# Performance work log

Measured on AMD Instinct MI355X. Metric: run time of the kernel, lower is better.

The kernel has to match this reference:

```python
import jax, jax.numpy as jnp
import numpy as np
from jax import lax

# dims
B, CH, CC, DG, H, W = 2, 256, 256, 8, 64, 64
KK = 3  # dcn kernel size
K = KK * KK
GN_GROUPS = 32
EPS = 1e-6


def conv2d(x, w, b, pad=0, groups=1):
    out = lax.conv_general_dilated(x, w, (1, 1), [(pad, pad), (pad, pad)],
                                   feature_group_count=groups)
    return out + b[None, :, None, None]


def group_norm(x, gamma, beta):
    b, c, h, w = x.shape
    xg = x.reshape(b, GN_GROUPS, c // GN_GROUPS, h, w)
    mu = xg.mean(axis=(2, 3, 4), keepdims=True)
    var = xg.var(axis=(2, 3, 4), keepdims=True)
    xn = ((xg - mu) * lax.rsqrt(var + EPS)).reshape(b, c, h, w)
    return xn * gamma[None, :, None, None] + beta[None, :, None, None]


def deform_conv2d(x, off_y, off_x, mask, weight, bias):
    # x: [B,C,H,W]; off_y/off_x/mask: [B,DG,K,H,W]; weight: [Cout,C,3,3]
    b, c, h, w = x.shape
    cg = c // DG
    offs = jnp.arange(KK, dtype=x.dtype) - (KK // 2)  # pad = 1, dilation = 1
    ky = jnp.repeat(offs, KK)  # [K]
    kx = jnp.tile(offs, KK)    # [K]
    base_y = ky[:, None, None] + jnp.arange(h, dtype=x.dtype)[None, :, None]  # [K,H,1]
    base_x = kx[:, None, None] + jnp.arange(w, dtype=x.dtype)[None, None, :]  # [K,1,W]
    py = base_y[None, None] + off_y  # [B,DG,K,H,W]
    px = base_x[None, None] + off_x
    y0f = jnp.floor(py)
    x0f = jnp.floor(px)
    wy1 = py - y0f
    wx1 = px - x0f
    y0 = y0f.astype(jnp.int32)
    x0 = x0f.astype(jnp.int32)
    xg = x.reshape(b, DG, cg, h * w)

    def gather(yi, xi, wt):
        valid = (yi >= 0) & (yi < h) & (xi >= 0) & (xi < w)  # zero padding outside
        idx = (jnp.clip(yi, 0, h - 1) * w + jnp.clip(xi, 0, w - 1)).reshape(b, DG, 1, K * h * w)
        g = jnp.take_along_axis(xg, idx, axis=3).reshape(b, DG, cg, K, h, w)
        return g * (wt * valid)[:, :, None]

    val = (gather(y0, x0, (1 - wy1) * (1 - wx1))
           + gather(y0, x0 + 1, (1 - wy1) * wx1)
           + gather(y0 + 1, x0, wy1 * (1 - wx1))
           + gather(y0 + 1, x0 + 1, wy1 * wx1))
    val = val * mask[:, :, None]  # modulated (DCNv2)
    w_r = weight.reshape(weight.shape[0], DG, cg, K)
    out = jnp.einsum('bgckhw,ogck->bohw', val, w_r)
    return out + bias[None, :, None, None]


def setup_inputs():
    key = jax.random.key(0)
    ks = jax.random.split(key, 32)
    s = 0.02
    inp = {
        'x_main': jax.random.normal(ks[0], (B, CH, H, W), jnp.float32),
        'prior': jax.random.normal(ks[1], (B, CC, 2 * H, 2 * W), jnp.float32),
        # downsample (bilinear resize + 3x3 conv)
        'w_ds': s * jax.random.normal(ks[2], (CC, CC, 3, 3), jnp.float32),
        'b_ds': jnp.zeros((CC,), jnp.float32),
        # offset_conv1: 1x1 -> GN -> SiLU -> depthwise 7x7 -> GN -> SiLU -> 1x1
        'w1': s * jax.random.normal(ks[3], (CH, CH + CC, 1, 1), jnp.float32),
        'b1': jnp.zeros((CH,), jnp.float32),
        'g1': jnp.ones((CH,), jnp.float32),
        'bt1': jnp.zeros((CH,), jnp.float32),
        'w_dw': s * jax.random.normal(ks[4], (CH, 1, 7, 7), jnp.float32),
        'b_dw': jnp.zeros((CH,), jnp.float32),
        'g2': jnp.ones((CH,), jnp.float32),
        'bt2': jnp.zeros((CH,), jnp.float32),
        'w2': s * jax.random.normal(ks[5], (CH, CH, 1, 1), jnp.float32),
        'b2': jnp.zeros((CH,), jnp.float32),
        # offset_conv2: 3x3 -> GN -> SiLU
        'w3': s * jax.random.normal(ks[6], (CH, CH, 3, 3), jnp.float32),
        'b3': jnp.zeros((CH,), jnp.float32),
        'g3': jnp.ones((CH,), jnp.float32),
        'bt3': jnp.zeros((CH,), jnp.float32),
        # dcn.conv_offset: 3x3 -> 3*DG*K channels (small init -> small offsets)
        'w_off': 0.01 * jax.random.normal(ks[7], (3 * DG * K, CH, 3, 3), jnp.float32),
        'b_off': jnp.zeros((3 * DG * K,), jnp.float32),
        # dcn main weight
        'w_dcn': s * jax.random.normal(ks[8], (CH, CH, 3, 3), jnp.float32),
        'b_dcn': jnp.zeros((CH,), jnp.float32),
    }
    return inp


def reference(x_main, prior, w_ds, b_ds, w1, b1, g1, bt1, w_dw, b_dw, g2, bt2,
              w2, b2, w3, b3, g3, bt3, w_off, b_off, w_dcn, b_dcn):
    b, c, h, w = x_main.shape
    # downsample prior to x_main resolution (bilinear, align_corners=False) + 3x3 conv
    pr = jax.image.resize(prior, (b, prior.shape[1], h, w), method='bilinear')
    pr = conv2d(pr, w_ds, b_ds, pad=1)
    # offset_conv1
    t = conv2d(jnp.concatenate([pr, x_main], axis=1), w1, b1, pad=0)
    t = jax.nn.silu(group_norm(t, g1, bt1))
    t = conv2d(t, w_dw, b_dw, pad=3, groups=c)  # depthwise 7x7
    t = jax.nn.silu(group_norm(t, g2, bt2))
    t = conv2d(t, w2, b2, pad=0)
    # offset_conv2 (previous_offset is None)
    offset_feat = jax.nn.silu(group_norm(conv2d(t, w3, b3, pad=1), g3, bt3))
    # DCNv2Pack: offsets/mask from offset_feat, sample x_main
    o = conv2d(offset_feat, w_off, b_off, pad=1)  # [B, 3*DG*K, H, W]
    o1, o2, m = jnp.split(o, 3, axis=1)
    off = jnp.concatenate([o1, o2], axis=1).reshape(b, DG, K, 2, h, w)
    off_y = off[:, :, :, 0]
    off_x = off[:, :, :, 1]
    mask = jax.nn.sigmoid(m).reshape(b, DG, K, h, w)
    warp_feat = deform_conv2d(x_main, off_y, off_x, mask, w_dcn, b_dcn)
    return warp_feat, offset_feat
```

## Files before the change

kernel.cpp:

```cpp
#include <hip/hip_runtime.h>
#include <math.h>


typedef __attribute__((ext_vector_type(8))) short short8;
typedef __attribute__((ext_vector_type(4))) float f32x4;
typedef unsigned short ushort_t;
typedef unsigned int uint_t;

__device__ __forceinline__ ushort_t f2bf(float f) {
  uint_t u = __float_as_uint(f);
  return (ushort_t)((u + 0x7fffu + ((u >> 16) & 1u)) >> 16);
}
__device__ __forceinline__ float bf2f(ushort_t h) {
  return __uint_as_float(((uint_t)h) << 16);
}
__device__ __forceinline__ uint_t pk2(float a, float b) {
  return (uint_t)f2bf(a) | ((uint_t)f2bf(b) << 16);
}

#define GLL(g, l) \
  __builtin_amdgcn_global_load_lds((const __attribute__((address_space(1))) void*)(const void*)(g), \
                                   (__attribute__((address_space(3))) void*)(void*)(l), 16, 0, 0)
#define WAITVM(n) __builtin_amdgcn_s_waitcnt(0x0F70 | (n))
#define CFENCE() asm volatile("" ::: "memory")

#define OFF_P1   0u
#define OFF_Y1   4460544u
#define OFF_Y2   8654848u
#define OFF_O    12849152u
#define OFF_WDS  16388096u
#define OFF_W1   17567744u
#define OFF_W2   17829888u
#define OFF_W3   17960960u
#define OFF_X    19140608u
#define OFF_WDW  23334912u
#define OFF_GNP  23385088u

__global__ __launch_bounds__(256) void k_down(const float* __restrict__ pr,
                                              ushort_t* __restrict__ out) {
  int idx = blockIdx.x * 256 + threadIdx.x;
  int x = idx & 63, y = (idx >> 6) & 63, bc = idx >> 12;
  const float* p = pr + (size_t)bc * 16384;
  const float w4[4] = {0.125f, 0.375f, 0.375f, 0.125f};
  float wy[4], wx[4];
  int ry[4], rx[4];
  float sy = 0.f, sx = 0.f;
#pragma unroll
  for (int t = 0; t < 4; ++t) {
    int yy = 2 * y - 1 + t;
    bool vy = (yy >= 0) && (yy < 128);
    wy[t] = vy ? w4[t] : 0.f; ry[t] = vy ? yy : 0; sy += wy[t];
    int xx = 2 * x - 1 + t;
    bool vx = (xx >= 0) && (xx < 128);
    wx[t] = vx ? w4[t] : 0.f; rx[t] = vx ? xx : 0; sx += wx[t];
  }
  float acc = 0.f;
#pragma unroll
  for (int t = 0; t < 4; ++t) {
    const float* rowp = p + ry[t] * 128;
    acc += wy[t] * (wx[0] * rowp[rx[0]] + wx[1] * rowp[rx[1]] +
                    wx[2] * rowp[rx[2]] + wx[3] * rowp[rx[3]]);
  }
  out[idx] = f2bf(acc / (sy * sx));
}

template <typename SrcT>
__global__ __launch_bounds__(256) void k_tr(const SrcT* __restrict__ src,
                                            ushort_t* __restrict__ dst,
                                            int pad) {
  __shared__ SrcT tile[64][65];
  int bx = blockIdx.x;
  int c4 = bx & 3, y = (bx >> 2) & 63, b = bx >> 8;
  int tid = threadIdx.x;
  int x = tid & 63, cl = tid >> 6;
#pragma unroll
  for (int i = 0; i < 16; ++i) {
    int c = (c4 << 6) + cl + (i << 2);
    tile[cl + (i << 2)][x] = src[(((size_t)(b * 256 + c)) << 12) + (y << 6) + x];
  }
  __syncthreads();
  int W = 64 + 2 * pad;
  int c2 = tid & 63, xq = tid >> 6;
#pragma unroll
  for (int i = 0; i < 16; ++i) {
    int x2 = xq + (i << 2);
    SrcT v = tile[c2][x2];
    ushort_t o;
    if constexpr (sizeof(SrcT) == 4) o = f2bf((float)v); else o = (ushort_t)v;
    dst[((size_t)((b * W + y + pad) * W + x2 + pad)) * 256 + (c4 << 6) + c2] = o;
  }
}

__global__ __launch_bounds__(256) void k_trnf(const ushort_t* __restrict__ src,
                                              float* __restrict__ dst) {
  __shared__ float tile[64][65];
  int bx = blockIdx.x;
  int cq = bx & 3, y = (bx >> 2) & 63, b = bx >> 8;
  int tid = threadIdx.x;
  int s8 = tid & 7, px = tid >> 3;
#pragma unroll
  for (int i = 0; i < 2; ++i) {
    int p = px + (i << 5);
    uint4 u = *(const uint4*)(src + ((size_t)((b * 66 + y + 1) * 66 + p + 1)) * 256 + (cq << 6) + (s8 << 3));
    uint_t w[4] = {u.x, u.y, u.z, u.w};
#pragma unroll
    for (int q = 0; q < 4; ++q) {
      tile[(s8 << 3) + 2 * q][p] = __uint_as_float(w[q] << 16);
      tile[(s8 << 3) + 2 * q + 1][p] = __uint_as_float(w[q] & 0xffff0000u);
    }
  }
  __syncthreads();
  int x2 = tid & 63, cl = tid >> 6;
#pragma unroll
  for (int i = 0; i < 16; ++i) {
    int c = cl + (i << 2);
    dst[((size_t)(b * 256 + (cq << 6) + c)) * 4096 + (y << 6) + x2] = tile[c][x2];
  }
}

__global__ __launch_bounds__(256) void k_wprep_all(
    const float* __restrict__ w_ds, const float* __restrict__ w1,
    const float* __restrict__ w2, const float* __restrict__ w3,
    const float* __restrict__ w_dw,
    ushort_t* __restrict__ Wds, ushort_t* __restrict__ W1,
    ushort_t* __restrict__ W2, ushort_t* __restrict__ W3,
    float* __restrict__ Wdw) {
  int i = blockIdx.x * 256 + threadIdx.x;
  if (i < 589824) {
    int tap = i >> 16, r = i & 65535, co = r >> 8, ci = r & 255;
    Wds[i] = f2bf(w_ds[((co << 8) + ci) * 9 + tap]);
  } else if (i < 720896) {
    int l = i - 589824;
    W1[l] = f2bf(w1[l]);
  } else if (i < 786432) {
    int l = i - 720896;
    W2[l] = f2bf(w2[l]);
  } else if (i < 1376256) {
    int l = i - 786432;
    int tap = l >> 16, r = l & 65535, co = r >> 8, ci = r & 255;
    W3[l] = f2bf(w3[((co << 8) + ci) * 9 + tap]);
  } else if (i < 1388800) {
    int l = i - 1376256;
    int t = l >> 8, c = l & 255;
    Wdw[l] = w_dw[c * 49 + t];
  }
}

__global__ __launch_bounds__(256) void k_wprep_off(const float* __restrict__ w_off,
                                                   ushort_t* __restrict__ Wof) {
  int i = blockIdx.x * 256 + threadIdx.x;
  int tap = i >> 16, r = i & 65535, co = r >> 8, ci = r & 255;
  Wof[i] = (co < 216) ? f2bf(w_off[((co << 8) + ci) * 9 + tap]) : (ushort_t)0;
}

__global__ __launch_bounds__(256) void k_wdcn(const float* __restrict__ w,
                                              ushort_t* __restrict__ Wd) {
  int i = blockIdx.x * 256 + threadIdx.x;
  int kk = i % 288;
  int rest = i / 288;
  int co = rest & 255, g = rest >> 8;
  int k = kk >> 5, c = kk & 31;
  Wd[i] = f2bf(w[(size_t)co * 2304 + (g * 32 + c) * 9 + k]);
}

template <int NTAPS, int CI>
__global__ __launch_bounds__(256) void k_convmfma(
    const ushort_t* __restrict__ srcA, const ushort_t* __restrict__ srcB,
    const ushort_t* __restrict__ wtp, const float* __restrict__ bias,
    float* __restrict__ outF,
    ushort_t* __restrict__ outB,
    ushort_t* __restrict__ outC16,
    int CO_real, int inH, int inW, int outW, int outPad) {
  const int gx = blockIdx.x;
  const int b = gx >> 6, y = gx & 63;
  const int cobase = blockIdx.y << 6;
  const int tid = threadIdx.x;
  const int wv = tid >> 6, lane = tid & 63;

  __shared__ __align__(16) char lds[24576];

  f32x4 acc[4];
#pragma unroll
  for (int ni = 0; ni < 4; ++ni) acc[ni] = (f32x4)0.f;

  const int sub = lane >> 2;
  const int oct = (lane & 3) ^ ((lane >> 3) & 3);

  auto stage = [&](int s, int bufidx) {
    int tap, chunk;
    if constexpr (NTAPS == 9) { tap = s >> 3; chunk = s & 7; }
    else { tap = 0; chunk = s; }
    char* lb = lds + bufidx * 8192;
    {
      int px = (wv << 4) + sub;
      int srow, scol;
      if constexpr (NTAPS == 9) { srow = y + tap / 3; scol = tap % 3 + px; }
      else { srow = y; scol = px; }
      const ushort_t* sp = srcA;
      int cil = chunk << 5;
      if constexpr (CI == 512) {
        if (chunk >= 8) { sp = srcB; cil = (chunk & 7) << 5; }
      }
      const ushort_t* g = sp + ((size_t)((b * inH + srow) * inW + scol) * 256 + cil + (oct << 3));
      GLL(g, lb + (wv << 10));
    }
    {
      int col = (wv << 4) + sub;
      const ushort_t* g = wtp + ((size_t)(tap * 256 + cobase + col) * CI + (chunk << 5) + (oct << 3));
      GLL(g, lb + 4096 + (wv << 10));
    }
  };

  const int NSTEP = NTAPS * (CI >> 5);
  stage(0, 0);
  stage(1, 1);

  const int r15 = lane & 15;
  const int xo = (((lane >> 4) ^ ((lane >> 1) & 3)) << 4);

  for (int s = 0; s < NSTEP; ++s) {
    if (s + 2 < NSTEP) stage(s + 2, (s + 2) % 3);
    if (s + 2 < NSTEP) WAITVM(4);
    else if (s + 1 < NSTEP) WAITVM(2);
    else WAITVM(0);
    CFENCE();
    __builtin_amdgcn_s_barrier();
    CFENCE();
    char* lb = lds + (s % 3) * 8192;
    short8 af = *(const short8*)(lb + 4096 + (((wv << 4) + r15) << 6) + xo);
#pragma unroll
    for (int ni = 0; ni < 4; ++ni) {
      short8 bfr = *(const short8*)(lb + (((ni << 4) + r15) << 6) + xo);
      acc[ni] = __builtin_amdgcn_mfma_f32_16x16x32_bf16(af, bfr, acc[ni], 0, 0, 0);
    }
    CFENCE();
    __builtin_amdgcn_s_barrier();
    CFENCE();
  }

  const int coq = (lane >> 4) << 2;
  const int outH = 64 + 2 * outPad;
  int co4 = cobase + (wv << 4) + coq;
  if (co4 < CO_real) {
    float4 bv = *(const float4*)(bias + co4);
#pragma unroll
    for (int ni = 0; ni < 4; ++ni) {
      int px = (ni << 4) + r15;
      f32x4 a = acc[ni];
      if (outF) {
        size_t e = ((size_t)(b * CO_real + co4)) * 4096 + (y << 6) + px;
        outF[e] = a[0] + bv.x;
        outF[e + 4096] = a[1] + bv.y;
        outF[e + 8192] = a[2] + bv.z;
        outF[e + 12288] = a[3] + bv.w;
      }
      if (outC16) {
        size_t e = ((size_t)(b * CO_real + co4)) * 4096 + (y << 6) + px;
        outC16[e] = f2bf(a[0] + bv.x);
        outC16[e + 4096] = f2bf(a[1] + bv.y);
        outC16[e + 8192] = f2bf(a[2] + bv.z);
        outC16[e + 12288] = f2bf(a[3] + bv.w);
      }
      if (outB) {
        size_t e = ((size_t)((b * outH + y + outPad) * outW + px + outPad)) * 256 + co4;
        uint2 u;
        u.x = pk2(a[0] + bv.x, a[1] + bv.y);
        u.y = pk2(a[2] + bv.z, a[3] + bv.w);
        *(uint2*)(outB + e) = u;
      }
    }
  }
}

__global__ __launch_bounds__(256) void k_gnstat(const ushort_t* __restrict__ in,
                                                float* __restrict__ part) {
  int bg = blockIdx.x;
  int tid = threadIdx.x;
  int slot = tid & 31, px0 = tid >> 5;
  const ushort_t* base = in + ((size_t)(bg << 6)) * 256 + (slot << 3);
  float s = 0.f, ss = 0.f;
#pragma unroll
  for (int i = 0; i < 8; ++i) {
    uint4 u = *(const uint4*)(base + (size_t)(px0 + (i << 3)) * 256);
    uint_t w[4] = {u.x, u.y, u.z, u.w};
#pragma unroll
    for (int q = 0; q < 4; ++q) {
      float f0 = __uint_as_float(w[q] << 16);
      float f1 = __uint_as_float(w[q] & 0xffff0000u);
      s += f0 + f1;
      ss += f0 * f0 + f1 * f1;
    }
  }
  s += __shfl_down(s, 32);
  ss += __shfl_down(ss, 32);
  __shared__ float ls[4][32][2];
  int wv = tid >> 6, lane = tid & 63;
  if (lane < 32) { ls[wv][lane][0] = s; ls[wv][lane][1] = ss; }
  __syncthreads();
  if (tid < 32) {
    float S = ls[0][tid][0] + ls[1][tid][0] + ls[2][tid][0] + ls[3][tid][0];
    float SS = ls[0][tid][1] + ls[1][tid][1] + ls[2][tid][1] + ls[3][tid][1];
    part[((size_t)bg * 32 + tid) * 2] = S;
    part[((size_t)bg * 32 + tid) * 2 + 1] = SS;
  }
}

__global__ __launch_bounds__(256) void k_gnapply(const ushort_t* __restrict__ in,
                                                 const float* __restrict__ part,
                                                 const float* __restrict__ gamma,
                                                 const float* __restrict__ beta,
                                                 ushort_t* __restrict__ outN,
                                                 int outW, int outPad) {
  int bg = blockIdx.x;
  int b = bg >> 6, y = bg & 63;
  int tid = threadIdx.x;
  __shared__ float stats[32][2];
  if (tid < 64) {
    int slot = tid & 31, which = tid >> 5;
    float a = 0.f;
    for (int r = 0; r < 64; ++r)
      a += part[((size_t)(((b << 6) + r) * 32 + slot)) * 2 + which];
    stats[slot][which] = a;
  }
  __syncthreads();
  int slot = tid & 31, px0 = tid >> 5;
  float mu = stats[slot][0] * (1.f / 32768.f);
  float var = stats[slot][1] * (1.f / 32768.f) - mu * mu;
  float rstd = rsqrtf(var + 1e-6f);
  int c0 = slot << 3;
  float gm[8], bt[8];
#pragma unroll
  for (int j = 0; j < 8; ++j) { gm[j] = gamma[c0 + j]; bt[j] = beta[c0 + j]; }
  const ushort_t* base = in + ((size_t)(bg << 6)) * 256 + c0;
#pragma unroll
  for (int i = 0; i < 8; ++i) {
    int px = px0 + (i << 3);
    uint4 u = *(const uint4*)(base + (size_t)px * 256);
    uint_t w[4] = {u.x, u.y, u.z, u.w};
    float o8[8];
#pragma unroll
    for (int q = 0; q < 4; ++q) {
      float f0 = __uint_as_float(w[q] << 16);
      float f1 = __uint_as_float(w[q] & 0xffff0000u);
      float v0 = (f0 - mu) * rstd * gm[2 * q] + bt[2 * q];
      float v1 = (f1 - mu) * rstd * gm[2 * q + 1] + bt[2 * q + 1];
      o8[2 * q] = v0 / (1.f + expf(-v0));
      o8[2 * q + 1] = v1 / (1.f + expf(-v1));
    }
    size_t e = ((size_t)((b * (64 + 2 * outPad) + y + outPad) * outW + px + outPad)) * 256 + c0;
    uint4 o;
    o.x = pk2(o8[0], o8[1]); o.y = pk2(o8[2], o8[3]);
    o.z = pk2(o8[4], o8[5]); o.w = pk2(o8[6], o8[7]);
    *(uint4*)(outN + e) = o;
  }
}

__global__ __launch_bounds__(256) void k_dw7_nhwc(const ushort_t* __restrict__ in,
                                                  const float* __restrict__ wdwT,
                                                  const float* __restrict__ bias,
                                                  ushort_t* __restrict__ out) {
  int tid = threadIdx.x;
  int oct = tid & 31, pxl = tid >> 5;
  int pxg = blockIdx.x * 8 + pxl;
  int b = pxg >> 12, rem = pxg & 4095, y = rem >> 6, x = rem & 63;
  float a[8];
  float4 b0 = *(const float4*)(bias + (oct << 3));
  float4 b1 = *(const float4*)(bias + (oct << 3) + 4);
  a[0] = b0.x; a[1] = b0.y; a[2] = b0.z; a[3] = b0.w;
  a[4] = b1.x; a[5] = b1.y; a[6] = b1.z; a[7] = b1.w;
#pragma unroll
  for (int ky = 0; ky < 7; ++ky) {
    int yy = y + ky - 3;
    if ((unsigned)yy >= 64u) continue;
#pragma unroll
    for (int kx = 0; kx < 7; ++kx) {
      int xx = x + kx - 3;
      if ((unsigned)xx >= 64u) continue;
      int t = ky * 7 + kx;
      uint4 u = *(const uint4*)(in + ((size_t)((b << 12) + (yy << 6) + xx)) * 256 + (oct << 3));
      float4 w0 = *(const float4*)(wdwT + (t << 8) + (oct << 3));
      float4 w1 = *(const float4*)(wdwT + (t << 8) + (oct << 3) + 4);
      uint_t ws[4] = {u.x, u.y, u.z, u.w};
      float f[8];
#pragma unroll
      for (int q = 0; q < 4; ++q) {
        f[2 * q] = __uint_as_float(ws[q] << 16);
        f[2 * q + 1] = __uint_as_float(ws[q] & 0xffff0000u);
      }
      a[0] += f[0] * w0.x; a[1] += f[1] * w0.y; a[2] += f[2] * w0.z; a[3] += f[3] * w0.w;
      a[4] += f[4] * w1.x; a[5] += f[5] * w1.y; a[6] += f[6] * w1.z; a[7] += f[7] * w1.w;
    }
  }
  uint4 o;
  o.x = pk2(a[0], a[1]); o.y = pk2(a[2], a[3]);
  o.z = pk2(a[4], a[5]); o.w = pk2(a[6], a[7]);
  *(uint4*)(out + ((size_t)pxg) * 256 + (oct << 3)) = o;
}

__global__ __launch_bounds__(256) void k_dcn_mfma(
    const ushort_t* __restrict__ xb,
    const ushort_t* __restrict__ o16,
    const ushort_t* __restrict__ Wd,
    const float* __restrict__ bias,
    float* __restrict__ out) {
  const int blk = blockIdx.x;
  const int b = blk >> 7;
  const int y = (blk >> 1) & 63;
  const int xh = blk & 1;
  const int tid = threadIdx.x;
  const int wv = tid >> 6, lane = tid & 63;
  const int r15 = lane & 15, oct = lane >> 4;

  __shared__ float gw[4][288];
  __shared__ int gi[4][288];
  __shared__ __align__(16) ushort_t val[32][296];

  f32x4 acc[4][2];
#pragma unroll
  for (int mi = 0; mi < 4; ++mi)
#pragma unroll
    for (int ni = 0; ni < 2; ++ni) acc[mi][ni] = (f32x4)0.f;

  const int spx = tid & 31;
  const int sslot = (tid >> 5) & 3;
  const int skh = tid >> 7;
  const size_t obase = (size_t)b * 216 * 4096;
  const int pxy0 = (y << 6) + (xh << 5);

  for (int g = 0; g < 8; ++g) {
    __syncthreads();
    for (int t = tid; t < 288; t += 256) {
      int k = t >> 5, px = t & 31;
      int pxy = pxy0 + px;
      float oy = bf2f(o16[obase + (size_t)(18 * g + 2 * k) * 4096 + pxy]);
      float ox = bf2f(o16[obase + (size_t)(18 * g + 2 * k + 1) * 4096 + pxy]);
      float mm = bf2f(o16[obase + (size_t)(144 + 9 * g + k) * 4096 + pxy]);
      float m = 1.f / (1.f + expf(-mm));
      float py = (float)(y + (k / 3) - 1) + oy;
      float pxf = (float)((xh << 5) + px + (k % 3) - 1) + ox;
      float y0f = floorf(py), x0f = floorf(pxf);
      float wy1 = py - y0f, wx1 = pxf - x0f;
      int y0 = (int)y0f, xi0 = (int)x0f;
      int y1 = y0 + 1, xi1 = xi0 + 1;
      float vy0 = (y0 >= 0 && y0 < 64) ? 1.f : 0.f;
      float vy1 = (y1 >= 0 && y1 < 64) ? 1.f : 0.f;
      float vx0 = (xi0 >= 0 && xi0 < 64) ? 1.f : 0.f;
      float vx1 = (xi1 >= 0 && xi1 < 64) ? 1.f : 0.f;
      int y0c = min(max(y0, 0), 63), y1c = min(max(y1, 0), 63);
      int x0c = min(max(xi0, 0), 63), x1c = min(max(xi1, 0), 63);
      float wy0 = 1.f - wy1, wx0 = 1.f - wx1;
      gw[0][t] = wy0 * wx0 * m * vy0 * vx0;
      gw[1][t] = wy0 * wx1 * m * vy0 * vx1;
      gw[2][t] = wy1 * wx0 * m * vy1 * vx0;
      gw[3][t] = wy1 * wx1 * m * vy1 * vx1;
      gi[0][t] = (y0c << 6) + x0c;
      gi[1][t] = (y0c << 6) + x1c;
      gi[2][t] = (y1c << 6) + x0c;
      gi[3][t] = (y1c << 6) + x1c;
    }
    __syncthreads();
    {
      const ushort_t* xg = xb + (((size_t)b << 12) << 8) + (g << 5) + (sslot << 3);
      for (int k = skh; k < 9; k += 2) {
        int t = (k << 5) + spx;
        float av[8];
#pragma unroll
        for (int j = 0; j < 8; ++j) av[j] = 0.f;
#pragma unroll
        for (int c4 = 0; c4 < 4; ++c4) {
          float wgt = gw[c4][t];
          uint4 u = *(const uint4*)(xg + (size_t)gi[c4][t] * 256);
          uint_t wsv[4] = {u.x, u.y, u.z, u.w};
#pragma unroll
          for (int q = 0; q < 4; ++q) {
            av[2 * q] += wgt * __uint_as_float(wsv[q] << 16);
            av[2 * q + 1] += wgt * __uint_as_float(wsv[q] & 0xffff0000u);
          }
        }
        uint4 o;
        o.x = pk2(av[0], av[1]); o.y = pk2(av[2], av[3]);
        o.z = pk2(av[4], av[5]); o.w = pk2(av[6], av[7]);
        *(uint4*)(&val[spx][(k << 5) + (sslot << 3)]) = o;
      }
    }
    __syncthreads();
    const ushort_t* wg = Wd + ((size_t)((g << 8) + (wv << 6))) * 288;
    short8 afn[4];
#pragma unroll
    for (int mi = 0; mi < 4; ++mi)
      afn[mi] = *(const short8*)(wg + (size_t)((mi << 4) + r15) * 288 + (oct << 3));
#pragma unroll
    for (int kc = 0; kc < 9; ++kc) {
      short8 afc[4];
#pragma unroll
      for (int mi = 0; mi < 4; ++mi) afc[mi] = afn[mi];
      if (kc < 8) {
#pragma unroll
        for (int mi = 0; mi < 4; ++mi)
          afn[mi] = *(const short8*)(wg + (size_t)((mi << 4) + r15) * 288 + ((kc + 1) << 5) + (oct << 3));
      }
      short8 bf0 = *(const short8*)(&val[r15][(kc << 5) + (oct << 3)]);
      short8 bf1 = *(const short8*)(&val[16 + r15][(kc << 5) + (oct << 3)]);
#pragma unroll
      for (int mi = 0; mi < 4; ++mi) {
        acc[mi][0] = __builtin_amdgcn_mfma_f32_16x16x32_bf16(afc[mi], bf0, acc[mi][0], 0, 0, 0);
        acc[mi][1] = __builtin_amdgcn_mfma_f32_16x16x32_bf16(afc[mi], bf1, acc[mi][1], 0, 0, 0);
      }
    }
  }
#pragma unroll
  for (int mi = 0; mi < 4; ++mi) {
    int co4 = (wv << 6) + (mi << 4) + (oct << 2);
    float4 bv = *(const float4*)(bias + co4);
#pragma unroll
    for (int ni = 0; ni < 2; ++ni) {
      int px = (xh << 5) + (ni << 4) + r15;
      f32x4 a = acc[mi][ni];
      size_t e = (((size_t)b << 8) + co4) * 4096 + (y << 6) + px;
      out[e] = a[0] + bv.x;
      out[e + 4096] = a[1] + bv.y;
      out[e + 8192] = a[2] + bv.z;
      out[e + 12288] = a[3] + bv.w;
    }
  }
}

extern "C" void kernel_launch(void* const* d_in, const int* in_sizes, int n_in,
                              void* d_out, int out_size, void* d_ws,
                              size_t ws_size, hipStream_t stream) {
  const float* x_main = (const float*)d_in[0];
  const float* prior = (const float*)d_in[1];
  const float* w_ds = (const float*)d_in[2];
  const float* b_ds = (const float*)d_in[3];
  const float* w1 = (const float*)d_in[4];
  const float* b1 = (const float*)d_in[5];
  const float* g1 = (const float*)d_in[6];
  const float* bt1 = (const float*)d_in[7];
  const float* w_dw = (const float*)d_in[8];
  const float* b_dw = (const float*)d_in[9];
  const float* g2 = (const float*)d_in[10];
  const float* bt2 = (const float*)d_in[11];
  const float* w2 = (const float*)d_in[12];
  const float* b2 = (const float*)d_in[13];
  const float* w3 = (const float*)d_in[14];
  const float* b3 = (const float*)d_in[15];
  const float* g3 = (const float*)d_in[16];
  const float* bt3 = (const float*)d_in[17];
  const float* w_off = (const float*)d_in[18];
  const float* b_off = (const float*)d_in[19];
  const float* w_dcn = (const float*)d_in[20];
  const float* b_dcn = (const float*)d_in[21];

  float* out = (float*)d_out;
  float* warp = out;
  float* offf = out + 2097152;

  char* ws = (char*)d_ws;
  ushort_t* P1 = (ushort_t*)(ws + OFF_P1);
  ushort_t* Y1 = (ushort_t*)(ws + OFF_Y1);
  ushort_t* Y2 = (ushort_t*)(ws + OFF_Y2);
  ushort_t* o16 = (ushort_t*)(ws + OFF_O);
  ushort_t* Wds = (ushort_t*)(ws + OFF_WDS);
  ushort_t* W1 = (ushort_t*)(ws + OFF_W1);
  ushort_t* W2 = (ushort_t*)(ws + OFF_W2);
  ushort_t* W3 = (ushort_t*)(ws + OFF_W3);
  ushort_t* xb = (ushort_t*)(ws + OFF_X);
  float* Wdw = (float*)(ws + OFF_WDW);
  float* gnp = (float*)(ws + OFF_GNP);
  ushort_t* Wof = Y1;
  ushort_t* Wd = Y1 + 589824;

  hipMemsetAsync(ws + OFF_P1, 0, 4460544, stream);
  k_wprep_all<<<5425, 256, 0, stream>>>(w_ds, w1, w2, w3, w_dw, Wds, W1, W2, W3, Wdw);
  k_down<<<8192, 256, 0, stream>>>(prior, Y2);
  k_tr<ushort_t><<<512, 256, 0, stream>>>(Y2, P1, 1);
  k_tr<float><<<512, 256, 0, stream>>>(x_main, xb, 0);
  k_convmfma<9, 256><<<dim3(128, 4), 256, 0, stream>>>(P1, nullptr, Wds, b_ds,
                                                       nullptr, Y1, nullptr, 256, 66, 66, 64, 0);
  k_convmfma<1, 512><<<dim3(128, 4), 256, 0, stream>>>(Y1, xb, W1, b1,
                                                       nullptr, Y2, nullptr, 256, 64, 64, 64, 0);
  k_gnstat<<<128, 256, 0, stream>>>(Y2, gnp);
  k_gnapply<<<128, 256, 0, stream>>>(Y2, gnp, g1, bt1, Y1, 64, 0);
  k_dw7_nhwc<<<1024, 256, 0, stream>>>(Y1, Wdw, b_dw, Y2);
  k_gnstat<<<128, 256, 0, stream>>>(Y2, gnp);
  k_gnapply<<<128, 256, 0, stream>>>(Y2, gnp, g2, bt2, Y1, 64, 0);
  k_convmfma<1, 256><<<dim3(128, 4), 256, 0, stream>>>(Y1, nullptr, W2, b2,
                                                       nullptr, P1, nullptr, 256, 64, 64, 66, 1);
  k_wprep_off<<<2304, 256, 0, stream>>>(w_off, Wof);
  k_wdcn<<<2304, 256, 0, stream>>>(w_dcn, Wd);
  k_convmfma<9, 256><<<dim3(128, 4), 256, 0, stream>>>(P1, nullptr, W3, b3,
                                                       nullptr, Y2, nullptr, 256, 66, 66, 64, 0);
  k_gnstat<<<128, 256, 0, stream>>>(Y2, gnp);
  k_gnapply<<<128, 256, 0, stream>>>(Y2, gnp, g3, bt3, P1, 66, 1);
  k_trnf<<<512, 256, 0, stream>>>(P1, offf);
  k_convmfma<9, 256><<<dim3(128, 4), 256, 0, stream>>>(P1, nullptr, Wof, b_off,
                                                       nullptr, nullptr, o16, 216, 66, 66, 64, 0);
  k_dcn_mfma<<<256, 256, 0, stream>>>(xb, o16, Wd, b_dcn, warp);
}
```

Measured before the change: 373.5 us.

## Restructure conv pipeline, fuse GN stats and downsample-transpose, split DCN output channels

```diff
diff --git a/kernel.cpp b/kernel.cpp
--- a/kernel.cpp
+++ b/kernel.cpp
@@ -35,12 +35,17 @@
 #define OFF_X    19140608u
 #define OFF_WDW  23334912u
 #define OFF_GNP  23385088u
-
-__global__ __launch_bounds__(256) void k_down(const float* __restrict__ pr,
-                                              ushort_t* __restrict__ out) {
-  int idx = blockIdx.x * 256 + threadIdx.x;
-  int x = idx & 63, y = (idx >> 6) & 63, bc = idx >> 12;
-  const float* p = pr + (size_t)bc * 16384;
+#define OFF_WOF  23417856u
+#define OFF_WD   24597504u
+
+__global__ __launch_bounds__(256) void k_down_nhwc(const float* __restrict__ pr,
+                                                   ushort_t* __restrict__ dst) {
+  int bx = blockIdx.x;
+  int cq = bx & 3, y = (bx >> 2) & 63, b = bx >> 8;
+  int tid = threadIdx.x;
+  int px = tid & 63, sub = tid >> 6;
+  int c0 = (cq << 6) + (sub << 4);
+
   const float w4[4] = {0.125f, 0.375f, 0.375f, 0.125f};
   float wy[4], wx[4];
   int ry[4], rx[4];
@@ -50,25 +55,33 @@
     int yy = 2 * y - 1 + t;
     bool vy = (yy >= 0) && (yy < 128);
     wy[t] = vy ? w4[t] : 0.f; ry[t] = vy ? yy : 0; sy += wy[t];
-    int xx = 2 * x - 1 + t;
+    int xx = 2 * px - 1 + t;
     bool vx = (xx >= 0) && (xx < 128);
     wx[t] = vx ? w4[t] : 0.f; rx[t] = vx ? xx : 0; sx += wx[t];
   }
-  float acc = 0.f;
-#pragma unroll
-  for (int t = 0; t < 4; ++t) {
-    const float* rowp = p + ry[t] * 128;
-    acc += wy[t] * (wx[0] * rowp[rx[0]] + wx[1] * rowp[rx[1]] +
-                    wx[2] * rowp[rx[2]] + wx[3] * rowp[rx[3]]);
-  }
-  out[idx] = f2bf(acc / (sy * sx));
-}
-
-template <typename SrcT>
-__global__ __launch_bounds__(256) void k_tr(const SrcT* __restrict__ src,
-                                            ushort_t* __restrict__ dst,
-                                            int pad) {
-  __shared__ SrcT tile[64][65];
+  float rn = 1.f / (sy * sx);
+
+  ushort_t o16[16];
+#pragma unroll
+  for (int i = 0; i < 16; ++i) {
+    const float* p = pr + (size_t)(b * 256 + c0 + i) * 16384;
+    float acc = 0.f;
+#pragma unroll
+    for (int t = 0; t < 4; ++t) {
+      const float* rp = p + ry[t] * 128;
+      acc += wy[t] * (wx[0] * rp[rx[0]] + wx[1] * rp[rx[1]] +
+                      wx[2] * rp[rx[2]] + wx[3] * rp[rx[3]]);
+    }
+    o16[i] = f2bf(acc * rn);
+  }
+  ushort_t* d = dst + ((size_t)((b * 66 + y + 1) * 66 + px + 1)) * 256 + c0;
+  *(uint4*)(d) = *(uint4*)(&o16[0]);
+  *(uint4*)(d + 8) = *(uint4*)(&o16[8]);
+}
+
+__global__ __launch_bounds__(256) void k_trf(const float* __restrict__ src,
+                                             ushort_t* __restrict__ dst) {
+  __shared__ float tile[64][65];
   int bx = blockIdx.x;
   int c4 = bx & 3, y = (bx >> 2) & 63, b = bx >> 8;
   int tid = threadIdx.x;
@@ -79,15 +92,11 @@
     tile[cl + (i << 2)][x] = src[(((size_t)(b * 256 + c)) << 12) + (y << 6) + x];
   }
   __syncthreads();
-  int W = 64 + 2 * pad;
   int c2 = tid & 63, xq = tid >> 6;
 #pragma unroll
   for (int i = 0; i < 16; ++i) {
     int x2 = xq + (i << 2);
-    SrcT v = tile[c2][x2];
-    ushort_t o;
-    if constexpr (sizeof(SrcT) == 4) o = f2bf((float)v); else o = (ushort_t)v;
-    dst[((size_t)((b * W + y + pad) * W + x2 + pad)) * 256 + (c4 << 6) + c2] = o;
+    dst[((size_t)((b * 64 + y) * 64 + x2)) * 256 + (c4 << 6) + c2] = f2bf(tile[c2][x2]);
   }
 }
 
@@ -121,10 +130,12 @@
 __global__ __launch_bounds__(256) void k_wprep_all(
     const float* __restrict__ w_ds, const float* __restrict__ w1,
     const float* __restrict__ w2, const float* __restrict__ w3,
-    const float* __restrict__ w_dw,
+    const float* __restrict__ w_dw, const float* __restrict__ w_off,
+    const float* __restrict__ w_dcn,
     ushort_t* __restrict__ Wds, ushort_t* __restrict__ W1,
     ushort_t* __restrict__ W2, ushort_t* __restrict__ W3,
-    float* __restrict__ Wdw) {
+    float* __restrict__ Wdw, ushort_t* __restrict__ Wof,
+    ushort_t* __restrict__ Wd) {
   int i = blockIdx.x * 256 + threadIdx.x;
   if (i < 589824) {
     int tap = i >> 16, r = i & 65535, co = r >> 8, ci = r & 255;
@@ -143,131 +154,142 @@
     int l = i - 1376256;
     int t = l >> 8, c = l & 255;
     Wdw[l] = w_dw[c * 49 + t];
-  }
-}
-
-__global__ __launch_bounds__(256) void k_wprep_off(const float* __restrict__ w_off,
-                                                   ushort_t* __restrict__ Wof) {
-  int i = blockIdx.x * 256 + threadIdx.x;
-  int tap = i >> 16, r = i & 65535, co = r >> 8, ci = r & 255;
-  Wof[i] = (co < 216) ? f2bf(w_off[((co << 8) + ci) * 9 + tap]) : (ushort_t)0;
-}
-
-__global__ __launch_bounds__(256) void k_wdcn(const float* __restrict__ w,
-                                              ushort_t* __restrict__ Wd) {
-  int i = blockIdx.x * 256 + threadIdx.x;
-  int kk = i % 288;
-  int rest = i / 288;
-  int co = rest & 255, g = rest >> 8;
-  int k = kk >> 5, c = kk & 31;
-  Wd[i] = f2bf(w[(size_t)co * 2304 + (g * 32 + c) * 9 + k]);
+  } else if (i < 1978624) {
+    int l = i - 1388800;
+    int tap = l >> 16, r = l & 65535, co = r >> 8, ci = r & 255;
+    Wof[l] = (co < 216) ? f2bf(w_off[((co << 8) + ci) * 9 + tap]) : (ushort_t)0;
+  } else if (i < 2568448) {
+    int l = i - 1978624;
+    int kk = l % 288;
+    int rest = l / 288;
+    int co = rest & 255, g = rest >> 8;
+    int k = kk >> 5, c = kk & 31;
+    Wd[l] = f2bf(w_dcn[(size_t)co * 2304 + (g * 32 + c) * 9 + k]);
+  }
 }
 
 template <int NTAPS, int CI>
 __global__ __launch_bounds__(256) void k_convmfma(
     const ushort_t* __restrict__ srcA, const ushort_t* __restrict__ srcB,
     const ushort_t* __restrict__ wtp, const float* __restrict__ bias,
-    float* __restrict__ outF,
     ushort_t* __restrict__ outB,
     ushort_t* __restrict__ outC16,
+    float* __restrict__ gnp,
     int CO_real, int inH, int inW, int outW, int outPad) {
   const int gx = blockIdx.x;
   const int b = gx >> 6, y = gx & 63;
   const int cobase = blockIdx.y << 6;
   const int tid = threadIdx.x;
   const int wv = tid >> 6, lane = tid & 63;
-
-  __shared__ __align__(16) char lds[24576];
+  const int r15 = lane & 15, oct = lane >> 4;
+
+  __shared__ __align__(16) char lds[2][32768];
 
   f32x4 acc[4];
 #pragma unroll
   for (int ni = 0; ni < 4; ++ni) acc[ni] = (f32x4)0.f;
 
-  const int sub = lane >> 2;
-  const int oct = (lane & 3) ^ ((lane >> 3) & 3);
-
-  auto stage = [&](int s, int bufidx) {
-    int tap, chunk;
-    if constexpr (NTAPS == 9) { tap = s >> 3; chunk = s & 7; }
-    else { tap = 0; chunk = s; }
-    char* lb = lds + bufidx * 8192;
-    {
-      int px = (wv << 4) + sub;
+  auto stage = [&](int s, int buf) {
+    int tap, ch;
+    if constexpr (NTAPS == 9) { tap = s >> 1; ch = s & 1; }
+    else { tap = 0; ch = s; }
+    char* lb = lds[buf];
+#pragma unroll
+    for (int q = 0; q < 4; ++q) {
+      int j = (wv << 2) + q;
+      int px = (j << 2) + (lane >> 4);
+      int u_log = (lane & 15) ^ (px & 7);
       int srow, scol;
-      if constexpr (NTAPS == 9) { srow = y + tap / 3; scol = tap % 3 + px; }
+      if constexpr (NTAPS == 9) { srow = y + tap / 3; scol = px + tap % 3; }
       else { srow = y; scol = px; }
       const ushort_t* sp = srcA;
-      int cil = chunk << 5;
+      int cil = ch << 7;
       if constexpr (CI == 512) {
-        if (chunk >= 8) { sp = srcB; cil = (chunk & 7) << 5; }
+        if (ch >= 2) { sp = srcB; cil = (ch - 2) << 7; }
       }
-      const ushort_t* g = sp + ((size_t)((b * inH + srow) * inW + scol) * 256 + cil + (oct << 3));
-      GLL(g, lb + (wv << 10));
-    }
-    {
-      int col = (wv << 4) + sub;
-      const ushort_t* g = wtp + ((size_t)(tap * 256 + cobase + col) * CI + (chunk << 5) + (oct << 3));
-      GLL(g, lb + 4096 + (wv << 10));
+      const ushort_t* g = sp + ((size_t)((b * inH + srow) * inW + scol) * 256 + cil + (u_log << 3));
+      GLL(g, lb + (j << 10));
+    }
+#pragma unroll
+    for (int q = 0; q < 4; ++q) {
+      int j = (wv << 2) + q;
+      int col = (j << 2) + (lane >> 4);
+      int u_log = (lane & 15) ^ (col & 7);
+      const ushort_t* g = wtp + ((size_t)(tap * 256 + cobase + col) * CI + (ch << 7) + (u_log << 3));
+      GLL(g, lb + 16384 + (j << 10));
     }
   };
 
-  const int NSTEP = NTAPS * (CI >> 5);
+  const int NSTEP = (NTAPS == 9) ? 18 : (CI >> 7);
   stage(0, 0);
-  stage(1, 1);
-
-  const int r15 = lane & 15;
-  const int xo = (((lane >> 4) ^ ((lane >> 1) & 3)) << 4);
 
   for (int s = 0; s < NSTEP; ++s) {
-    if (s + 2 < NSTEP) stage(s + 2, (s + 2) % 3);
-    if (s + 2 < NSTEP) WAITVM(4);
-    else if (s + 1 < NSTEP) WAITVM(2);
+    if (s + 1 < NSTEP) stage(s + 1, (s + 1) & 1);
+    if (s + 1 < NSTEP) WAITVM(8);
     else WAITVM(0);
     CFENCE();
     __builtin_amdgcn_s_barrier();
     CFENCE();
-    char* lb = lds + (s % 3) * 8192;
-    short8 af = *(const short8*)(lb + 4096 + (((wv << 4) + r15) << 6) + xo);
-#pragma unroll
-    for (int ni = 0; ni < 4; ++ni) {
-      short8 bfr = *(const short8*)(lb + (((ni << 4) + r15) << 6) + xo);
-      acc[ni] = __builtin_amdgcn_mfma_f32_16x16x32_bf16(af, bfr, acc[ni], 0, 0, 0);
-    }
+    const char* lb = lds[s & 1];
+    __builtin_amdgcn_s_setprio(1);
+#pragma unroll
+    for (int kc = 0; kc < 4; ++kc) {
+      int u_rd = (((kc << 2) + oct) ^ (r15 & 7)) << 4;
+      short8 af = *(const short8*)(lb + 16384 + (((wv << 4) + r15) << 8) + u_rd);
+#pragma unroll
+      for (int ni = 0; ni < 4; ++ni) {
+        short8 bfr = *(const short8*)(lb + (((ni << 4) + r15) << 8) + u_rd);
+        acc[ni] = __builtin_amdgcn_mfma_f32_16x16x32_bf16(af, bfr, acc[ni], 0, 0, 0);
+      }
+    }
+    __builtin_amdgcn_s_setprio(0);
     CFENCE();
     __builtin_amdgcn_s_barrier();
     CFENCE();
   }
 
-  const int coq = (lane >> 4) << 2;
+  const int coq = oct << 2;
   const int outH = 64 + 2 * outPad;
   int co4 = cobase + (wv << 4) + coq;
+  float s_l = 0.f, ss_l = 0.f;
   if (co4 < CO_real) {
     float4 bv = *(const float4*)(bias + co4);
 #pragma unroll
     for (int ni = 0; ni < 4; ++ni) {
       int px = (ni << 4) + r15;
       f32x4 a = acc[ni];
-      if (outF) {
-        size_t e = ((size_t)(b * CO_real + co4)) * 4096 + (y << 6) + px;
-        outF[e] = a[0] + bv.x;
-        outF[e + 4096] = a[1] + bv.y;
-        outF[e + 8192] = a[2] + bv.z;
-        outF[e + 12288] = a[3] + bv.w;
+      float v0 = a[0] + bv.x, v1 = a[1] + bv.y, v2 = a[2] + bv.z, v3 = a[3] + bv.w;
+      if (gnp) {
+        s_l += v0 + v1 + v2 + v3;
+        ss_l += v0 * v0 + v1 * v1 + v2 * v2 + v3 * v3;
       }
       if (outC16) {
         size_t e = ((size_t)(b * CO_real + co4)) * 4096 + (y << 6) + px;
-        outC16[e] = f2bf(a[0] + bv.x);
-        outC16[e + 4096] = f2bf(a[1] + bv.y);
-        outC16[e + 8192] = f2bf(a[2] + bv.z);
-        outC16[e + 12288] = f2bf(a[3] + bv.w);
+        outC16[e] = f2bf(v0);
+        outC16[e + 4096] = f2bf(v1);
+        outC16[e + 8192] = f2bf(v2);
+        outC16[e + 12288] = f2bf(v3);
       }
       if (outB) {
         size_t e = ((size_t)((b * outH + y + outPad) * outW + px + outPad)) * 256 + co4;
         uint2 u;
-        u.x = pk2(a[0] + bv.x, a[1] + bv.y);
-        u.y = pk2(a[2] + bv.z, a[3] + bv.w);
+        u.x = pk2(v0, v1);
+        u.y = pk2(v2, v3);
         *(uint2*)(outB + e) = u;
       }
+    }
+  }
+  if (gnp) {
+#pragma unroll
+    for (int m = 1; m <= 16; m <<= 1) {
+      s_l += __shfl_xor(s_l, m);
+      ss_l += __shfl_xor(ss_l, m);
+    }
+    if ((lane & 31) == 0) {
+      int slot = (cobase >> 3) + (wv << 1) + (lane >> 5);
+      float* p = gnp + ((size_t)((b << 6) + y) * 32 + slot) * 2;
+      p[0] = s_l;
+      p[1] = ss_l;
     }
   }
 }
@@ -407,6 +429,7 @@
   const int b = blk >> 7;
   const int y = (blk >> 1) & 63;
   const int xh = blk & 1;
+  const int coh = blockIdx.y;
   const int tid = threadIdx.x;
   const int wv = tid >> 6, lane = tid & 63;
   const int r15 = lane & 15, oct = lane >> 4;
@@ -415,9 +438,9 @@
   __shared__ int gi[4][288];
   __shared__ __align__(16) ushort_t val[32][296];
 
-  f32x4 acc[4][2];
-#pragma unroll
-  for (int mi = 0; mi < 4; ++mi)
+  f32x4 acc[2][2];
+#pragma unroll
+  for (int mi = 0; mi < 2; ++mi)
 #pragma unroll
     for (int ni = 0; ni < 2; ++ni) acc[mi][ni] = (f32x4)0.f;
 
@@ -460,7 +483,7 @@
     }
     __syncthreads();
     {
-      const ushort_t* xg = xb + (((size_t)b << 12) << 8) + (g << 5) + (sslot << 3);
+      const ushort_t* xg = xb + ((size_t)b << 20) + (g << 5) + (sslot << 3);
       for (int k = skh; k < 9; k += 2) {
         int t = (k << 5) + spx;
         float av[8];
@@ -484,33 +507,24 @@
       }
     }
     __syncthreads();
-    const ushort_t* wg = Wd + ((size_t)((g << 8) + (wv << 6))) * 288;
-    short8 afn[4];
-#pragma unroll
-    for (int mi = 0; mi < 4; ++mi)
-      afn[mi] = *(const short8*)(wg + (size_t)((mi << 4) + r15) * 288 + (oct << 3));
+    const ushort_t* wg = Wd + ((size_t)((g << 8) + (coh << 7) + (wv << 5))) * 288;
+    __builtin_amdgcn_s_setprio(1);
 #pragma unroll
     for (int kc = 0; kc < 9; ++kc) {
-      short8 afc[4];
-#pragma unroll
-      for (int mi = 0; mi < 4; ++mi) afc[mi] = afn[mi];
-      if (kc < 8) {
-#pragma unroll
-        for (int mi = 0; mi < 4; ++mi)
-          afn[mi] = *(const short8*)(wg + (size_t)((mi << 4) + r15) * 288 + ((kc + 1) << 5) + (oct << 3));
-      }
+      short8 af0 = *(const short8*)(wg + (size_t)r15 * 288 + (kc << 5) + (oct << 3));
+      short8 af1 = *(const short8*)(wg + (size_t)(16 + r15) * 288 + (kc << 5) + (oct << 3));
       short8 bf0 = *(const short8*)(&val[r15][(kc << 5) + (oct << 3)]);
       short8 bf1 = *(const short8*)(&val[16 + r15][(kc << 5) + (oct << 3)]);
-#pragma unroll
-      for (int mi = 0; mi < 4; ++mi) {
-        acc[mi][0] = __builtin_amdgcn_mfma_f32_16x16x32_bf16(afc[mi], bf0, acc[mi][0], 0, 0, 0);
-        acc[mi][1] = __builtin_amdgcn_mfma_f32_16x16x32_bf16(afc[mi], bf1, acc[mi][1], 0, 0, 0);
-      }
-    }
-  }
-#pragma unroll
-  for (int mi = 0; mi < 4; ++mi) {
-    int co4 = (wv << 6) + (mi << 4) + (oct << 2);
+      acc[0][0] = __builtin_amdgcn_mfma_f32_16x16x32_bf16(af0, bf0, acc[0][0], 0, 0, 0);
+      acc[0][1] = __builtin_amdgcn_mfma_f32_16x16x32_bf16(af0, bf1, acc[0][1], 0, 0, 0);
+      acc[1][0] = __builtin_amdgcn_mfma_f32_16x16x32_bf16(af1, bf0, acc[1][0], 0, 0, 0);
+      acc[1][1] = __builtin_amdgcn_mfma_f32_16x16x32_bf16(af1, bf1, acc[1][1], 0, 0, 0);
+    }
+    __builtin_amdgcn_s_setprio(0);
+  }
+#pragma unroll
+  for (int mi = 0; mi < 2; ++mi) {
+    int co4 = (coh << 7) + (wv << 5) + (mi << 4) + (oct << 2);
     float4 bv = *(const float4*)(bias + co4);
 #pragma unroll
     for (int ni = 0; ni < 2; ++ni) {
@@ -567,33 +581,29 @@
   ushort_t* xb = (ushort_t*)(ws + OFF_X);
   float* Wdw = (float*)(ws + OFF_WDW);
   float* gnp = (float*)(ws + OFF_GNP);
-  ushort_t* Wof = Y1;
-  ushort_t* Wd = Y1 + 589824;
-
-  hipMemsetAsync(ws + OFF_P1, 0, 4460544, stream);
-  k_wprep_all<<<5425, 256, 0, stream>>>(w_ds, w1, w2, w3, w_dw, Wds, W1, W2, W3, Wdw);
-  k_down<<<8192, 256, 0, stream>>>(prior, Y2);
-  k_tr<ushort_t><<<512, 256, 0, stream>>>(Y2, P1, 1);
-  k_tr<float><<<512, 256, 0, stream>>>(x_main, xb, 0);
+  ushort_t* Wof = (ushort_t*)(ws + OFF_WOF);
+  ushort_t* Wd = (ushort_t*)(ws + OFF_WD);
+
+  (void)hipMemsetAsync(ws + OFF_P1, 0, 4460544, stream);
+  k_wprep_all<<<10033, 256, 0, stream>>>(w_ds, w1, w2, w3, w_dw, w_off, w_dcn,
+                                         Wds, W1, W2, W3, Wdw, Wof, Wd);
+  k_down_nhwc<<<512, 256, 0, stream>>>(prior, P1);
+  k_trf<<<512, 256, 0, stream>>>(x_main, xb);
   k_convmfma<9, 256><<<dim3(128, 4), 256, 0, stream>>>(P1, nullptr, Wds, b_ds,
-                                                       nullptr, Y1, nullptr, 256, 66, 66, 64, 0);
+                                                       Y1, nullptr, nullptr, 256, 66, 66, 64, 0);
   k_convmfma<1, 512><<<dim3(128, 4), 256, 0, stream>>>(Y1, xb, W1, b1,
-                                                       nullptr, Y2, nullptr, 256, 64, 64, 64, 0);
-  k_gnstat<<<128, 256, 0, stream>>>(Y2, gnp);
+                                                       Y2, nullptr, gnp, 256, 64, 64, 64, 0);
   k_gnapply<<<128, 256, 0, stream>>>(Y2, gnp, g1, bt1, Y1, 64, 0);
   k_dw7_nhwc<<<1024, 256, 0, stream>>>(Y1, Wdw, b_dw, Y2);
   k_gnstat<<<128, 256, 0, stream>>>(Y2, gnp);
   k_gnapply<<<128, 256, 0, stream>>>(Y2, gnp, g2, bt2, Y1, 64, 0);
   k_convmfma<1, 256><<<dim3(128, 4), 256, 0, stream>>>(Y1, nullptr, W2, b2,
-                                                       nullptr, P1, nullptr, 256, 64, 64, 66, 1);
-  k_wprep_off<<<2304, 256, 0, stream>>>(w_off, Wof);
-  k_wdcn<<<2304, 256, 0, stream>>>(w_dcn, Wd);
+                                                       P1, nullptr, nullptr, 256, 64, 64, 66, 1);
   k_convmfma<9, 256><<<dim3(128, 4), 256, 0, stream>>>(P1, nullptr, W3, b3,
-                                                       nullptr, Y2, nullptr, 256, 66, 66, 64, 0);
-  k_gnstat<<<128, 256, 0, stream>>>(Y2, gnp);
+                                                       Y2, nullptr, gnp, 256, 66, 66, 64, 0);
   k_gnapply<<<128, 256, 0, stream>>>(Y2, gnp, g3, bt3, P1, 66, 1);
   k_trnf<<<512, 256, 0, stream>>>(P1, offf);
   k_convmfma<9, 256><<<dim3(128, 4), 256, 0, stream>>>(P1, nullptr, Wof, b_off,
-                                                       nullptr, nullptr, o16, 216, 66, 66, 64, 0);
-  k_dcn_mfma<<<256, 256, 0, stream>>>(xb, o16, Wd, b_dcn, warp);
-}
+                                                       nullptr, o16, nullptr, 216, 66, 66, 64, 0);
+  k_dcn_mfma<<<dim3(256, 2), 256, 0, stream>>>(xb, o16, Wd, b_dcn, warp);
+}
```

Result: faster. 338.4 us (-9.4%).
